# Kernel optimization log

Hardware: AMD Instinct MI355X
Metric: run time of the kernel (lower is better)

## Reference

```python
import jax, jax.numpy as jnp
import numpy as np


def setup_inputs() -> dict:
    key = jax.random.key(0)
    ks = jax.random.split(key, 5)
    B, S, D, E, H = 8, 4096, 512, 4, 64
    x = jax.random.normal(ks[0], (B, S, D), dtype=jnp.float32)
    router_w = jax.random.normal(ks[1], (D, E), dtype=jnp.float32) * 0.02
    router_b = jnp.zeros((E,), dtype=jnp.float32)
    w1 = jax.random.normal(ks[2], (E, D, H), dtype=jnp.float32) * 0.02
    b1 = jnp.zeros((E, H), dtype=jnp.float32)
    w2 = jax.random.normal(ks[3], (E, H, D), dtype=jnp.float32) * 0.02
    b2 = jnp.zeros((E, D), dtype=jnp.float32)
    return {"x": x, "router_w": router_w, "router_b": router_b,
            "w1": w1, "b1": b1, "w2": w2, "b2": b2}


def reference(x, router_w, router_b, w1, b1, w2, b2):
    # Router: softmax over experts. weights: [B, S, E]
    weights = jax.nn.softmax(jnp.einsum('bsd,de->bse', x, router_w) + router_b, axis=-1)
    # All experts run densely on every token (batched over the E axis).
    # h: [B, S, E, H]; TF Dense(activation='gelu') uses exact (non-tanh) gelu.
    h = jax.nn.gelu(jnp.einsum('bsd,edh->bseh', x, w1) + b1, approximate=False)
    # expert outputs: [B, S, E, D]; Dropout is identity at inference.
    expert_out = jnp.einsum('bseh,ehd->bsed', h, w2) + b2
    # weighted sum over experts -> [B, S, D]
    return jnp.sum(expert_out * weights[..., None], axis=2)
```

## Files before the change

kernel.cpp:

```cpp
#include <hip/hip_runtime.h>
#include <hip/hip_bf16.h>
#include <math.h>


typedef short v8s __attribute__((ext_vector_type(8)));
typedef float v4f __attribute__((ext_vector_type(4)));

#define XS 520
#define HS 296

__device__ __forceinline__ unsigned short f2bf(float f) {
    unsigned int u = __builtin_bit_cast(unsigned int, f);
    u += 0x7fffu + ((u >> 16) & 1u);
    return (unsigned short)(u >> 16);
}

__global__ void moe_prep(const float* __restrict__ w1,
                         const float* __restrict__ w2,
                         const float* __restrict__ b2,
                         const float* __restrict__ rw,
                         unsigned short* __restrict__ w1p,
                         unsigned short* __restrict__ w2p,
                         unsigned short* __restrict__ rp) {
    int idx = blockIdx.x * 256 + threadIdx.x;
    if (idx < 131072) {
        int block = idx >> 9, within = idx & 511;
        int kb = block >> 4, cb = block & 15;
        int n = within >> 5, kl = within & 31;
        int k = kb * 32 + kl;
        int col = cb * 16 + n;
        int e = col >> 6, h = col & 63;
        w1p[idx] = f2bf(w1[(e * 512 + k) * 64 + h]);
    } else if (idx < 131072 + 147456) {
        int op = idx - 131072;
        int block = op >> 9, within = op & 511;
        int kb = block >> 5, cb = block & 31;
        int n = within >> 5, kl = within & 31;
        int k = kb * 32 + kl;
        int d = cb * 16 + n;
        float v = 0.f;
        if (k < 256) {
            int e = k >> 6, h = k & 63;
            v = w2[(e * 64 + h) * 512 + d];
        } else if (k < 260) {
            v = b2[(k - 256) * 512 + d];
        }
        w2p[op] = f2bf(v);
    } else if (idx < 131072 + 147456 + 8192) {
        int op = idx - (131072 + 147456);
        int kb = op >> 9, within = op & 511;
        int n = within >> 5, kl = within & 31;
        int k = kb * 32 + kl;
        float v = (n < 4) ? rw[k * 4 + n] : 0.f;
        rp[op] = f2bf(v);
    }
}

__global__ __launch_bounds__(256, 2)
void moe_main(const float* __restrict__ x,
              const float* __restrict__ rb,
              const float* __restrict__ b1,
              const unsigned short* __restrict__ w1p,
              const unsigned short* __restrict__ w2p,
              const unsigned short* __restrict__ rp,
              float* __restrict__ out) {
    __shared__ __align__(16) unsigned short lx[64 * XS];
    __shared__ float llog[64 * 4];
    __shared__ float lw[64 * 4];

    const int tid  = threadIdx.x;
    const int lane = tid & 63, wv = tid >> 6;
    const int lr = lane & 15, lq = lane >> 4;
    const long t0 = (long)blockIdx.x * 64;

    const float4* xt = (const float4*)(x + t0 * 512);
    #pragma unroll
    for (int it = 0; it < 32; ++it) {
        int F = it * 256 + tid;
        int row = F >> 7, c4 = F & 127;
        float4 v = xt[F];
        unsigned int p0 = (unsigned int)f2bf(v.x) | ((unsigned int)f2bf(v.y) << 16);
        unsigned int p1 = (unsigned int)f2bf(v.z) | ((unsigned int)f2bf(v.w) << 16);
        *(uint2*)&lx[row * XS + c4 * 4] = make_uint2(p0, p1);
    }
    __syncthreads();

    {
        v4f accR; accR[0] = accR[1] = accR[2] = accR[3] = 0.f;
        #pragma unroll
        for (int kb = 0; kb < 16; ++kb) {
            v8s a = *(const v8s*)(const void*)&lx[(16 * wv + lr) * XS + kb * 32 + lq * 8];
            v8s b = *(const v8s*)(const void*)&rp[kb * 512 + lr * 32 + lq * 8];
            accR = __builtin_amdgcn_mfma_f32_16x16x32_bf16(a, b, accR, 0, 0, 0);
        }
        if (lr < 4) {
            #pragma unroll
            for (int r = 0; r < 4; ++r)
                llog[(16 * wv + lq * 4 + r) * 4 + lr] = accR[r];
        }
    }
    __syncthreads();
    if (tid < 64) {
        float l[4];
        #pragma unroll
        for (int e = 0; e < 4; ++e) l[e] = llog[tid * 4 + e] + rb[e];
        float mx = fmaxf(fmaxf(l[0], l[1]), fmaxf(l[2], l[3]));
        float ex[4], s = 0.f;
        #pragma unroll
        for (int e = 0; e < 4; ++e) { ex[e] = expf(l[e] - mx); s += ex[e]; }
        float inv = 1.f / s;
        #pragma unroll
        for (int e = 0; e < 4; ++e) lw[tid * 4 + e] = ex[e] * inv;
    }
    __syncthreads();

    v4f acc1[4][4];
    #pragma unroll
    for (int mt = 0; mt < 4; ++mt)
        #pragma unroll
        for (int nt = 0; nt < 4; ++nt)
            acc1[mt][nt][0] = acc1[mt][nt][1] = acc1[mt][nt][2] = acc1[mt][nt][3] = 0.f;

    for (int kb = 0; kb < 16; ++kb) {
        v8s a[4], b[4];
        #pragma unroll
        for (int mt = 0; mt < 4; ++mt)
            a[mt] = *(const v8s*)(const void*)&lx[(16 * mt + lr) * XS + kb * 32 + lq * 8];
        #pragma unroll
        for (int nt = 0; nt < 4; ++nt)
            b[nt] = *(const v8s*)(const void*)&w1p[(size_t)(kb * 16 + wv * 4 + nt) * 512 + lr * 32 + lq * 8];
        #pragma unroll
        for (int mt = 0; mt < 4; ++mt)
            #pragma unroll
            for (int nt = 0; nt < 4; ++nt)
                acc1[mt][nt] = __builtin_amdgcn_mfma_f32_16x16x32_bf16(a[mt], b[nt], acc1[mt][nt], 0, 0, 0);
    }
    __syncthreads();

    {
        float b1v[4];
        #pragma unroll
        for (int nt = 0; nt < 4; ++nt) b1v[nt] = b1[wv * 64 + nt * 16 + lr];
        #pragma unroll
        for (int mt = 0; mt < 4; ++mt) {
            #pragma unroll
            for (int r = 0; r < 4; ++r) {
                int row = 16 * mt + lq * 4 + r;
                float wt = lw[row * 4 + wv];
                #pragma unroll
                for (int nt = 0; nt < 4; ++nt) {
                    float v = acc1[mt][nt][r] + b1v[nt];
                    float g = 0.5f * v * (1.f + erff(v * 0.70710678118f)) * wt;
                    lx[row * HS + wv * 64 + nt * 16 + lr] = f2bf(g);
                }
            }
        }
        int r = tid >> 2, e = tid & 3;
        lx[r * HS + 256 + e] = f2bf(lw[tid]);
        #pragma unroll
        for (int i = 0; i < 7; ++i)
            lx[r * HS + 260 + e + 4 * i] = 0;
    }
    __syncthreads();

    v4f acc2[4][8];
    #pragma unroll
    for (int mt = 0; mt < 4; ++mt)
        #pragma unroll
        for (int nt = 0; nt < 8; ++nt)
            acc2[mt][nt][0] = acc2[mt][nt][1] = acc2[mt][nt][2] = acc2[mt][nt][3] = 0.f;

    for (int kb = 0; kb < 9; ++kb) {
        v8s a[4], b[8];
        #pragma unroll
        for (int mt = 0; mt < 4; ++mt)
            a[mt] = *(const v8s*)(const void*)&lx[(16 * mt + lr) * HS + kb * 32 + lq * 8];
        #pragma unroll
        for (int nt = 0; nt < 8; ++nt)
            b[nt] = *(const v8s*)(const void*)&w2p[(size_t)(kb * 32 + wv * 8 + nt) * 512 + lr * 32 + lq * 8];
        #pragma unroll
        for (int mt = 0; mt < 4; ++mt)
            #pragma unroll
            for (int nt = 0; nt < 8; ++nt)
                acc2[mt][nt] = __builtin_amdgcn_mfma_f32_16x16x32_bf16(a[mt], b[nt], acc2[mt][nt], 0, 0, 0);
    }

    float* ot = out + t0 * 512;
    #pragma unroll
    for (int mt = 0; mt < 4; ++mt)
        #pragma unroll
        for (int nt = 0; nt < 8; ++nt)
            #pragma unroll
            for (int r = 0; r < 4; ++r) {
                int row = 16 * mt + lq * 4 + r;
                int col = 128 * wv + 16 * nt + lr;
                ot[row * 512 + col] = acc2[mt][nt][r];
            }
}

extern "C" void kernel_launch(void* const* d_in, const int* in_sizes, int n_in,
                              void* d_out, int out_size, void* d_ws, size_t ws_size,
                              hipStream_t stream) {
    const float* x  = (const float*)d_in[0];
    const float* rw = (const float*)d_in[1];
    const float* rb = (const float*)d_in[2];
    const float* w1 = (const float*)d_in[3];
    const float* b1 = (const float*)d_in[4];
    const float* w2 = (const float*)d_in[5];
    const float* b2 = (const float*)d_in[6];

    unsigned short* w1p = (unsigned short*)d_ws;
    unsigned short* w2p = w1p + 131072;
    unsigned short* rp  = w2p + 147456;

    moe_prep<<<1120, 256, 0, stream>>>(w1, w2, b2, rw, w1p, w2p, rp);
    moe_main<<<512, 256, 0, stream>>>(x, rb, b1, w1p, w2p, rp, (float*)d_out);
}
```

Baseline: 142.6 us.

## Halve token tile to 32 rows and fuse router GEMM into expert-1 loop

```diff
diff --git a/kernel.cpp b/kernel.cpp
--- a/kernel.cpp
+++ b/kernel.cpp
@@ -56,7 +56,7 @@
     }
 }
 
-__global__ __launch_bounds__(256, 2)
+__global__ __launch_bounds__(256, 4)
 void moe_main(const float* __restrict__ x,
               const float* __restrict__ rb,
               const float* __restrict__ b1,
@@ -64,18 +64,17 @@
               const unsigned short* __restrict__ w2p,
               const unsigned short* __restrict__ rp,
               float* __restrict__ out) {
-    __shared__ __align__(16) unsigned short lx[64 * XS];
-    __shared__ float llog[64 * 4];
-    __shared__ float lw[64 * 4];
+    __shared__ __align__(16) unsigned short lx[32 * XS];
+    __shared__ float lw[32 * 4];
 
     const int tid  = threadIdx.x;
     const int lane = tid & 63, wv = tid >> 6;
     const int lr = lane & 15, lq = lane >> 4;
-    const long t0 = (long)blockIdx.x * 64;
+    const long t0 = (long)blockIdx.x * 32;
 
     const float4* xt = (const float4*)(x + t0 * 512);
     #pragma unroll
-    for (int it = 0; it < 32; ++it) {
+    for (int it = 0; it < 16; ++it) {
         int F = it * 256 + tid;
         int row = F >> 7, c4 = F & 127;
         float4 v = xt[F];
@@ -85,56 +84,64 @@
     }
     __syncthreads();
 
-    {
-        v4f accR; accR[0] = accR[1] = accR[2] = accR[3] = 0.f;
-        #pragma unroll
-        for (int kb = 0; kb < 16; ++kb) {
-            v8s a = *(const v8s*)(const void*)&lx[(16 * wv + lr) * XS + kb * 32 + lq * 8];
-            v8s b = *(const v8s*)(const void*)&rp[kb * 512 + lr * 32 + lq * 8];
-            accR = __builtin_amdgcn_mfma_f32_16x16x32_bf16(a, b, accR, 0, 0, 0);
-        }
-        if (lr < 4) {
-            #pragma unroll
-            for (int r = 0; r < 4; ++r)
-                llog[(16 * wv + lq * 4 + r) * 4 + lr] = accR[r];
-        }
-    }
-    __syncthreads();
-    if (tid < 64) {
-        float l[4];
-        #pragma unroll
-        for (int e = 0; e < 4; ++e) l[e] = llog[tid * 4 + e] + rb[e];
-        float mx = fmaxf(fmaxf(l[0], l[1]), fmaxf(l[2], l[3]));
-        float ex[4], s = 0.f;
-        #pragma unroll
-        for (int e = 0; e < 4; ++e) { ex[e] = expf(l[e] - mx); s += ex[e]; }
-        float inv = 1.f / s;
-        #pragma unroll
-        for (int e = 0; e < 4; ++e) lw[tid * 4 + e] = ex[e] * inv;
-    }
-    __syncthreads();
-
-    v4f acc1[4][4];
-    #pragma unroll
-    for (int mt = 0; mt < 4; ++mt)
+    v4f acc1[2][4];
+    v4f accR[2];
+    #pragma unroll
+    for (int mt = 0; mt < 2; ++mt) {
+        accR[mt][0] = accR[mt][1] = accR[mt][2] = accR[mt][3] = 0.f;
         #pragma unroll
         for (int nt = 0; nt < 4; ++nt)
             acc1[mt][nt][0] = acc1[mt][nt][1] = acc1[mt][nt][2] = acc1[mt][nt][3] = 0.f;
+    }
 
     for (int kb = 0; kb < 16; ++kb) {
-        v8s a[4], b[4];
-        #pragma unroll
-        for (int mt = 0; mt < 4; ++mt)
+        v8s a[2], b[4], br;
+        #pragma unroll
+        for (int mt = 0; mt < 2; ++mt)
             a[mt] = *(const v8s*)(const void*)&lx[(16 * mt + lr) * XS + kb * 32 + lq * 8];
         #pragma unroll
         for (int nt = 0; nt < 4; ++nt)
             b[nt] = *(const v8s*)(const void*)&w1p[(size_t)(kb * 16 + wv * 4 + nt) * 512 + lr * 32 + lq * 8];
-        #pragma unroll
-        for (int mt = 0; mt < 4; ++mt)
+        br = *(const v8s*)(const void*)&rp[kb * 512 + lr * 32 + lq * 8];
+        #pragma unroll
+        for (int mt = 0; mt < 2; ++mt) {
             #pragma unroll
             for (int nt = 0; nt < 4; ++nt)
                 acc1[mt][nt] = __builtin_amdgcn_mfma_f32_16x16x32_bf16(a[mt], b[nt], acc1[mt][nt], 0, 0, 0);
-    }
+            accR[mt] = __builtin_amdgcn_mfma_f32_16x16x32_bf16(a[mt], br, accR[mt], 0, 0, 0);
+        }
+    }
+
+    float wreg[2][4];
+    {
+        float rbv = rb[lane & 3];
+        #pragma unroll
+        for (int mt = 0; mt < 2; ++mt)
+            #pragma unroll
+            for (int r = 0; r < 4; ++r) {
+                float v = accR[mt][r] + rbv;
+                float m = fmaxf(v, __shfl_xor(v, 1));
+                m = fmaxf(m, __shfl_xor(m, 2));
+                float e = expf(v - m);
+                float s = e + __shfl_xor(e, 1);
+                s += __shfl_xor(s, 2);
+                wreg[mt][r] = e / s;
+            }
+    }
+    if (wv == 0 && lr < 4) {
+        #pragma unroll
+        for (int mt = 0; mt < 2; ++mt)
+            #pragma unroll
+            for (int r = 0; r < 4; ++r)
+                lw[(16 * mt + lq * 4 + r) * 4 + lr] = wreg[mt][r];
+    }
+    float wt[2][4];
+    #pragma unroll
+    for (int mt = 0; mt < 2; ++mt)
+        #pragma unroll
+        for (int r = 0; r < 4; ++r)
+            wt[mt][r] = __shfl(wreg[mt][r], (lane & 48) | wv);
+
     __syncthreads();
 
     {
@@ -142,44 +149,45 @@
         #pragma unroll
         for (int nt = 0; nt < 4; ++nt) b1v[nt] = b1[wv * 64 + nt * 16 + lr];
         #pragma unroll
-        for (int mt = 0; mt < 4; ++mt) {
+        for (int mt = 0; mt < 2; ++mt) {
             #pragma unroll
             for (int r = 0; r < 4; ++r) {
                 int row = 16 * mt + lq * 4 + r;
-                float wt = lw[row * 4 + wv];
                 #pragma unroll
                 for (int nt = 0; nt < 4; ++nt) {
                     float v = acc1[mt][nt][r] + b1v[nt];
-                    float g = 0.5f * v * (1.f + erff(v * 0.70710678118f)) * wt;
+                    float g = 0.5f * v * (1.f + erff(v * 0.70710678118f)) * wt[mt][r];
                     lx[row * HS + wv * 64 + nt * 16 + lr] = f2bf(g);
                 }
             }
         }
-        int r = tid >> 2, e = tid & 3;
-        lx[r * HS + 256 + e] = f2bf(lw[tid]);
-        #pragma unroll
-        for (int i = 0; i < 7; ++i)
-            lx[r * HS + 260 + e + 4 * i] = 0;
+        if (tid < 128) {
+            int r = tid >> 2, e = tid & 3;
+            lx[r * HS + 256 + e] = f2bf(lw[tid]);
+            #pragma unroll
+            for (int i = 0; i < 7; ++i)
+                lx[r * HS + 260 + e + 4 * i] = 0;
+        }
     }
     __syncthreads();
 
-    v4f acc2[4][8];
-    #pragma unroll
-    for (int mt = 0; mt < 4; ++mt)
+    v4f acc2[2][8];
+    #pragma unroll
+    for (int mt = 0; mt < 2; ++mt)
         #pragma unroll
         for (int nt = 0; nt < 8; ++nt)
             acc2[mt][nt][0] = acc2[mt][nt][1] = acc2[mt][nt][2] = acc2[mt][nt][3] = 0.f;
 
     for (int kb = 0; kb < 9; ++kb) {
-        v8s a[4], b[8];
-        #pragma unroll
-        for (int mt = 0; mt < 4; ++mt)
+        v8s a[2], b[8];
+        #pragma unroll
+        for (int mt = 0; mt < 2; ++mt)
             a[mt] = *(const v8s*)(const void*)&lx[(16 * mt + lr) * HS + kb * 32 + lq * 8];
         #pragma unroll
         for (int nt = 0; nt < 8; ++nt)
             b[nt] = *(const v8s*)(const void*)&w2p[(size_t)(kb * 32 + wv * 8 + nt) * 512 + lr * 32 + lq * 8];
         #pragma unroll
-        for (int mt = 0; mt < 4; ++mt)
+        for (int mt = 0; mt < 2; ++mt)
             #pragma unroll
             for (int nt = 0; nt < 8; ++nt)
                 acc2[mt][nt] = __builtin_amdgcn_mfma_f32_16x16x32_bf16(a[mt], b[nt], acc2[mt][nt], 0, 0, 0);
@@ -187,7 +195,7 @@
 
     float* ot = out + t0 * 512;
     #pragma unroll
-    for (int mt = 0; mt < 4; ++mt)
+    for (int mt = 0; mt < 2; ++mt)
         #pragma unroll
         for (int nt = 0; nt < 8; ++nt)
             #pragma unroll
@@ -214,5 +222,5 @@
     unsigned short* rp  = w2p + 147456;
 
     moe_prep<<<1120, 256, 0, stream>>>(w1, w2, b2, rw, w1p, w2p, rp);
-    moe_main<<<512, 256, 0, stream>>>(x, rb, b1, w1p, w2p, rp, (float*)d_out);
-}
+    moe_main<<<1024, 256, 0, stream>>>(x, rb, b1, w1p, w2p, rp, (float*)d_out);
+}
```

After: 170.1 us. 19.3% more time.

## Double threads per block, split expert tiles across 8 waves, fuse router softmax

Applied to the files above, without the earlier changes.

```diff
diff --git a/kernel.cpp b/kernel.cpp
--- a/kernel.cpp
+++ b/kernel.cpp
@@ -56,7 +56,7 @@
     }
 }
 
-__global__ __launch_bounds__(256, 2)
+__global__ __launch_bounds__(512, 4)
 void moe_main(const float* __restrict__ x,
               const float* __restrict__ rb,
               const float* __restrict__ b1,
@@ -65,7 +65,6 @@
               const unsigned short* __restrict__ rp,
               float* __restrict__ out) {
     __shared__ __align__(16) unsigned short lx[64 * XS];
-    __shared__ float llog[64 * 4];
     __shared__ float lw[64 * 4];
 
     const int tid  = threadIdx.x;
@@ -75,8 +74,8 @@
 
     const float4* xt = (const float4*)(x + t0 * 512);
     #pragma unroll
-    for (int it = 0; it < 32; ++it) {
-        int F = it * 256 + tid;
+    for (int it = 0; it < 16; ++it) {
+        int F = it * 512 + tid;
         int row = F >> 7, c4 = F & 127;
         float4 v = xt[F];
         unsigned int p0 = (unsigned int)f2bf(v.x) | ((unsigned int)f2bf(v.y) << 16);
@@ -85,103 +84,101 @@
     }
     __syncthreads();
 
+    v4f acc1[4][2];
+    v4f accR;
+    accR[0] = accR[1] = accR[2] = accR[3] = 0.f;
+    #pragma unroll
+    for (int mt = 0; mt < 4; ++mt)
+        #pragma unroll
+        for (int nt = 0; nt < 2; ++nt)
+            acc1[mt][nt][0] = acc1[mt][nt][1] = acc1[mt][nt][2] = acc1[mt][nt][3] = 0.f;
+
+    for (int kb = 0; kb < 16; ++kb) {
+        v8s a[4], b[2];
+        #pragma unroll
+        for (int mt = 0; mt < 4; ++mt)
+            a[mt] = *(const v8s*)(const void*)&lx[(16 * mt + lr) * XS + kb * 32 + lq * 8];
+        #pragma unroll
+        for (int nt = 0; nt < 2; ++nt)
+            b[nt] = *(const v8s*)(const void*)&w1p[(size_t)(kb * 16 + 2 * wv + nt) * 512 + lr * 32 + lq * 8];
+        if (wv < 4) {
+            v8s ar = *(const v8s*)(const void*)&lx[(16 * wv + lr) * XS + kb * 32 + lq * 8];
+            v8s br = *(const v8s*)(const void*)&rp[kb * 512 + lr * 32 + lq * 8];
+            accR = __builtin_amdgcn_mfma_f32_16x16x32_bf16(ar, br, accR, 0, 0, 0);
+        }
+        #pragma unroll
+        for (int mt = 0; mt < 4; ++mt)
+            #pragma unroll
+            for (int nt = 0; nt < 2; ++nt)
+                acc1[mt][nt] = __builtin_amdgcn_mfma_f32_16x16x32_bf16(a[mt], b[nt], acc1[mt][nt], 0, 0, 0);
+    }
+
+    if (wv < 4) {
+        float rbv = rb[lane & 3];
+        #pragma unroll
+        for (int r = 0; r < 4; ++r) {
+            float v = accR[r] + rbv;
+            float m = fmaxf(v, __shfl_xor(v, 1));
+            m = fmaxf(m, __shfl_xor(m, 2));
+            float e = expf(v - m);
+            float s = e + __shfl_xor(e, 1);
+            s += __shfl_xor(s, 2);
+            if (lr < 4)
+                lw[(16 * wv + lq * 4 + r) * 4 + lr] = e / s;
+        }
+    }
+
+    __syncthreads();
+
     {
-        v4f accR; accR[0] = accR[1] = accR[2] = accR[3] = 0.f;
-        #pragma unroll
-        for (int kb = 0; kb < 16; ++kb) {
-            v8s a = *(const v8s*)(const void*)&lx[(16 * wv + lr) * XS + kb * 32 + lq * 8];
-            v8s b = *(const v8s*)(const void*)&rp[kb * 512 + lr * 32 + lq * 8];
-            accR = __builtin_amdgcn_mfma_f32_16x16x32_bf16(a, b, accR, 0, 0, 0);
-        }
-        if (lr < 4) {
-            #pragma unroll
-            for (int r = 0; r < 4; ++r)
-                llog[(16 * wv + lq * 4 + r) * 4 + lr] = accR[r];
-        }
-    }
-    __syncthreads();
-    if (tid < 64) {
-        float l[4];
-        #pragma unroll
-        for (int e = 0; e < 4; ++e) l[e] = llog[tid * 4 + e] + rb[e];
-        float mx = fmaxf(fmaxf(l[0], l[1]), fmaxf(l[2], l[3]));
-        float ex[4], s = 0.f;
-        #pragma unroll
-        for (int e = 0; e < 4; ++e) { ex[e] = expf(l[e] - mx); s += ex[e]; }
-        float inv = 1.f / s;
-        #pragma unroll
-        for (int e = 0; e < 4; ++e) lw[tid * 4 + e] = ex[e] * inv;
-    }
-    __syncthreads();
-
-    v4f acc1[4][4];
-    #pragma unroll
-    for (int mt = 0; mt < 4; ++mt)
-        #pragma unroll
-        for (int nt = 0; nt < 4; ++nt)
-            acc1[mt][nt][0] = acc1[mt][nt][1] = acc1[mt][nt][2] = acc1[mt][nt][3] = 0.f;
-
-    for (int kb = 0; kb < 16; ++kb) {
-        v8s a[4], b[4];
-        #pragma unroll
-        for (int mt = 0; mt < 4; ++mt)
-            a[mt] = *(const v8s*)(const void*)&lx[(16 * mt + lr) * XS + kb * 32 + lq * 8];
-        #pragma unroll
-        for (int nt = 0; nt < 4; ++nt)
-            b[nt] = *(const v8s*)(const void*)&w1p[(size_t)(kb * 16 + wv * 4 + nt) * 512 + lr * 32 + lq * 8];
-        #pragma unroll
-        for (int mt = 0; mt < 4; ++mt)
-            #pragma unroll
-            for (int nt = 0; nt < 4; ++nt)
-                acc1[mt][nt] = __builtin_amdgcn_mfma_f32_16x16x32_bf16(a[mt], b[nt], acc1[mt][nt], 0, 0, 0);
-    }
-    __syncthreads();
-
-    {
-        float b1v[4];
-        #pragma unroll
-        for (int nt = 0; nt < 4; ++nt) b1v[nt] = b1[wv * 64 + nt * 16 + lr];
+        const int e = wv >> 1;
+        float b1v[2];
+        #pragma unroll
+        for (int nt = 0; nt < 2; ++nt)
+            b1v[nt] = b1[e * 64 + 32 * (wv & 1) + 16 * nt + lr];
         #pragma unroll
         for (int mt = 0; mt < 4; ++mt) {
             #pragma unroll
             for (int r = 0; r < 4; ++r) {
                 int row = 16 * mt + lq * 4 + r;
-                float wt = lw[row * 4 + wv];
+                float wt = lw[row * 4 + e];
                 #pragma unroll
-                for (int nt = 0; nt < 4; ++nt) {
+                for (int nt = 0; nt < 2; ++nt) {
                     float v = acc1[mt][nt][r] + b1v[nt];
                     float g = 0.5f * v * (1.f + erff(v * 0.70710678118f)) * wt;
-                    lx[row * HS + wv * 64 + nt * 16 + lr] = f2bf(g);
+                    lx[row * HS + 32 * wv + 16 * nt + lr] = f2bf(g);
                 }
             }
         }
-        int r = tid >> 2, e = tid & 3;
-        lx[r * HS + 256 + e] = f2bf(lw[tid]);
-        #pragma unroll
-        for (int i = 0; i < 7; ++i)
-            lx[r * HS + 260 + e + 4 * i] = 0;
+        if (tid < 256) {
+            int r = tid >> 2, e4 = tid & 3;
+            lx[r * HS + 256 + e4] = f2bf(lw[r * 4 + e4]);
+            #pragma unroll
+            for (int i = 0; i < 7; ++i)
+                lx[r * HS + 260 + e4 + 4 * i] = 0;
+        }
     }
     __syncthreads();
 
-    v4f acc2[4][8];
+    v4f acc2[4][4];
     #pragma unroll
     for (int mt = 0; mt < 4; ++mt)
         #pragma unroll
-        for (int nt = 0; nt < 8; ++nt)
+        for (int nt = 0; nt < 4; ++nt)
             acc2[mt][nt][0] = acc2[mt][nt][1] = acc2[mt][nt][2] = acc2[mt][nt][3] = 0.f;
 
     for (int kb = 0; kb < 9; ++kb) {
-        v8s a[4], b[8];
+        v8s a[4], b[4];
         #pragma unroll
         for (int mt = 0; mt < 4; ++mt)
             a[mt] = *(const v8s*)(const void*)&lx[(16 * mt + lr) * HS + kb * 32 + lq * 8];
         #pragma unroll
-        for (int nt = 0; nt < 8; ++nt)
-            b[nt] = *(const v8s*)(const void*)&w2p[(size_t)(kb * 32 + wv * 8 + nt) * 512 + lr * 32 + lq * 8];
-        #pragma unroll
-        for (int mt = 0; mt < 4; ++mt)
-            #pragma unroll
-            for (int nt = 0; nt < 8; ++nt)
+        for (int nt = 0; nt < 4; ++nt)
+            b[nt] = *(const v8s*)(const void*)&w2p[(size_t)(kb * 32 + 4 * wv + nt) * 512 + lr * 32 + lq * 8];
+        #pragma unroll
+        for (int mt = 0; mt < 4; ++mt)
+            #pragma unroll
+            for (int nt = 0; nt < 4; ++nt)
                 acc2[mt][nt] = __builtin_amdgcn_mfma_f32_16x16x32_bf16(a[mt], b[nt], acc2[mt][nt], 0, 0, 0);
     }
 
@@ -189,11 +186,11 @@
     #pragma unroll
     for (int mt = 0; mt < 4; ++mt)
         #pragma unroll
-        for (int nt = 0; nt < 8; ++nt)
+        for (int nt = 0; nt < 4; ++nt)
             #pragma unroll
             for (int r = 0; r < 4; ++r) {
                 int row = 16 * mt + lq * 4 + r;
-                int col = 128 * wv + 16 * nt + lr;
+                int col = 64 * wv + 16 * nt + lr;
                 ot[row * 512 + col] = acc2[mt][nt][r];
             }
 }
@@ -214,5 +211,5 @@
     unsigned short* rp  = w2p + 147456;
 
     moe_prep<<<1120, 256, 0, stream>>>(w1, w2, b2, rw, w1p, w2p, rp);
-    moe_main<<<512, 256, 0, stream>>>(x, rb, b1, w1p, w2p, rp, (float*)d_out);
-}
+    moe_main<<<512, 512, 0, stream>>>(x, rb, b1, w1p, w2p, rp, (float*)d_out);
+}
```

New measurement: 156.5 us. +9.7%, slower.

## Overlap second half of x staging with GEMM1 and fuse router into it

Applied to the files above, without the earlier changes.

```diff
diff --git a/kernel.cpp b/kernel.cpp
--- a/kernel.cpp
+++ b/kernel.cpp
@@ -65,7 +65,6 @@
               const unsigned short* __restrict__ rp,
               float* __restrict__ out) {
     __shared__ __align__(16) unsigned short lx[64 * XS];
-    __shared__ float llog[64 * 4];
     __shared__ float lw[64 * 4];
 
     const int tid  = threadIdx.x;
@@ -74,54 +73,37 @@
     const long t0 = (long)blockIdx.x * 64;
 
     const float4* xt = (const float4*)(x + t0 * 512);
-    #pragma unroll
-    for (int it = 0; it < 32; ++it) {
+
+    #pragma unroll
+    for (int it = 0; it < 16; ++it) {
         int F = it * 256 + tid;
-        int row = F >> 7, c4 = F & 127;
-        float4 v = xt[F];
+        int row = F >> 6, c = F & 63;
+        float4 v = xt[row * 128 + c];
         unsigned int p0 = (unsigned int)f2bf(v.x) | ((unsigned int)f2bf(v.y) << 16);
         unsigned int p1 = (unsigned int)f2bf(v.z) | ((unsigned int)f2bf(v.w) << 16);
-        *(uint2*)&lx[row * XS + c4 * 4] = make_uint2(p0, p1);
-    }
-    __syncthreads();
-
-    {
-        v4f accR; accR[0] = accR[1] = accR[2] = accR[3] = 0.f;
-        #pragma unroll
-        for (int kb = 0; kb < 16; ++kb) {
-            v8s a = *(const v8s*)(const void*)&lx[(16 * wv + lr) * XS + kb * 32 + lq * 8];
-            v8s b = *(const v8s*)(const void*)&rp[kb * 512 + lr * 32 + lq * 8];
-            accR = __builtin_amdgcn_mfma_f32_16x16x32_bf16(a, b, accR, 0, 0, 0);
-        }
-        if (lr < 4) {
-            #pragma unroll
-            for (int r = 0; r < 4; ++r)
-                llog[(16 * wv + lq * 4 + r) * 4 + lr] = accR[r];
-        }
-    }
-    __syncthreads();
-    if (tid < 64) {
-        float l[4];
-        #pragma unroll
-        for (int e = 0; e < 4; ++e) l[e] = llog[tid * 4 + e] + rb[e];
-        float mx = fmaxf(fmaxf(l[0], l[1]), fmaxf(l[2], l[3]));
-        float ex[4], s = 0.f;
-        #pragma unroll
-        for (int e = 0; e < 4; ++e) { ex[e] = expf(l[e] - mx); s += ex[e]; }
-        float inv = 1.f / s;
-        #pragma unroll
-        for (int e = 0; e < 4; ++e) lw[tid * 4 + e] = ex[e] * inv;
+        *(uint2*)&lx[row * XS + c * 4] = make_uint2(p0, p1);
     }
     __syncthreads();
 
     v4f acc1[4][4];
+    v4f accR;
+    accR[0] = accR[1] = accR[2] = accR[3] = 0.f;
     #pragma unroll
     for (int mt = 0; mt < 4; ++mt)
         #pragma unroll
         for (int nt = 0; nt < 4; ++nt)
             acc1[mt][nt][0] = acc1[mt][nt][1] = acc1[mt][nt][2] = acc1[mt][nt][3] = 0.f;
 
-    for (int kb = 0; kb < 16; ++kb) {
+    for (int kb = 0; kb < 8; ++kb) {
+        #pragma unroll
+        for (int s = 0; s < 2; ++s) {
+            int F = (kb * 2 + s) * 256 + tid;
+            int row = F >> 6, c = 64 + (F & 63);
+            float4 v = xt[row * 128 + c];
+            unsigned int p0 = (unsigned int)f2bf(v.x) | ((unsigned int)f2bf(v.y) << 16);
+            unsigned int p1 = (unsigned int)f2bf(v.z) | ((unsigned int)f2bf(v.w) << 16);
+            *(uint2*)&lx[row * XS + c * 4] = make_uint2(p0, p1);
+        }
         v8s a[4], b[4];
         #pragma unroll
         for (int mt = 0; mt < 4; ++mt)
@@ -129,11 +111,48 @@
         #pragma unroll
         for (int nt = 0; nt < 4; ++nt)
             b[nt] = *(const v8s*)(const void*)&w1p[(size_t)(kb * 16 + wv * 4 + nt) * 512 + lr * 32 + lq * 8];
+        v8s ar = *(const v8s*)(const void*)&lx[(16 * wv + lr) * XS + kb * 32 + lq * 8];
+        v8s br = *(const v8s*)(const void*)&rp[kb * 512 + lr * 32 + lq * 8];
+        accR = __builtin_amdgcn_mfma_f32_16x16x32_bf16(ar, br, accR, 0, 0, 0);
         #pragma unroll
         for (int mt = 0; mt < 4; ++mt)
             #pragma unroll
             for (int nt = 0; nt < 4; ++nt)
                 acc1[mt][nt] = __builtin_amdgcn_mfma_f32_16x16x32_bf16(a[mt], b[nt], acc1[mt][nt], 0, 0, 0);
+    }
+    __syncthreads();
+
+    for (int kb = 8; kb < 16; ++kb) {
+        v8s a[4], b[4];
+        #pragma unroll
+        for (int mt = 0; mt < 4; ++mt)
+            a[mt] = *(const v8s*)(const void*)&lx[(16 * mt + lr) * XS + kb * 32 + lq * 8];
+        #pragma unroll
+        for (int nt = 0; nt < 4; ++nt)
+            b[nt] = *(const v8s*)(const void*)&w1p[(size_t)(kb * 16 + wv * 4 + nt) * 512 + lr * 32 + lq * 8];
+        v8s ar = *(const v8s*)(const void*)&lx[(16 * wv + lr) * XS + kb * 32 + lq * 8];
+        v8s br = *(const v8s*)(const void*)&rp[kb * 512 + lr * 32 + lq * 8];
+        accR = __builtin_amdgcn_mfma_f32_16x16x32_bf16(ar, br, accR, 0, 0, 0);
+        #pragma unroll
+        for (int mt = 0; mt < 4; ++mt)
+            #pragma unroll
+            for (int nt = 0; nt < 4; ++nt)
+                acc1[mt][nt] = __builtin_amdgcn_mfma_f32_16x16x32_bf16(a[mt], b[nt], acc1[mt][nt], 0, 0, 0);
+    }
+
+    {
+        float rbv = rb[lane & 3];
+        #pragma unroll
+        for (int r = 0; r < 4; ++r) {
+            float v = accR[r] + rbv;
+            float m = fmaxf(v, __shfl_xor(v, 1));
+            m = fmaxf(m, __shfl_xor(m, 2));
+            float e = expf(v - m);
+            float s = e + __shfl_xor(e, 1);
+            s += __shfl_xor(s, 2);
+            if (lr < 4)
+                lw[(16 * wv + lq * 4 + r) * 4 + lr] = e / s;
+        }
     }
     __syncthreads();
 
```

After: 144.6 us. No clear change (+1.4%).
